# Kernel tuning notes

Hardware: AMD Instinct MI355X
Metric: run time of the kernel (lower is better)

## Reference

```python
import jax, jax.numpy as jnp
import numpy as np

B, L = 4096, 200
G_DIM, L_DIM, A_DIM, H = 64, 64, 8, 32
MAX_ACTION = 1.0


def _init(k, shape, fan_in):
    bound = 1.0 / np.sqrt(fan_in)
    return jax.random.uniform(k, shape, jnp.float32, -bound, bound)


def setup_inputs() -> dict:
    key = jax.random.key(0)
    ks = jax.random.split(key, 16)
    return dict(
        global_states=jax.random.normal(ks[0], (B, G_DIM), jnp.float32),
        local_states=jax.random.normal(ks[1], (B, L, L_DIM), jnp.float32),
        W_w=_init(ks[2], (H, G_DIM), G_DIM), W_b=_init(ks[3], (H,), G_DIM),
        U_w=_init(ks[4], (H, L_DIM), L_DIM), U_b=_init(ks[5], (H,), L_DIM),
        att_w=_init(ks[6], (1, 2 * H), 2 * H), att_b=_init(ks[7], (1,), 2 * H),
        l1_w=_init(ks[8], (256, 2 * H), 2 * H), l1_b=_init(ks[9], (256,), 2 * H),
        l2_w=_init(ks[10], (256, 256), 256), l2_b=_init(ks[11], (256,), 256),
        l3_w=_init(ks[12], (A_DIM, 256), 256), l3_b=_init(ks[13], (A_DIM,), 256),
    )


def reference(global_states, local_states, W_w, W_b, U_w, U_b,
              att_w, att_b, l1_w, l1_b, l2_w, l2_b, l3_w, l3_b):
    h = W_w.shape[0]  # 32
    wg = global_states @ W_w.T + W_b                              # [B,H]
    ul = jnp.einsum('bld,hd->blh', local_states, U_w) + U_b       # [B,L,H]
    # att input row0 = cat(wg, wg); rows 1..L = cat(wg, ul)
    a_g, a_l = att_w[0, :h], att_w[0, h:]
    g_term = wg @ a_g                                             # [B]
    s0 = jax.nn.leaky_relu(g_term + wg @ a_l + att_b[0])          # [B]
    sl = jax.nn.leaky_relu(g_term[:, None] + ul @ a_l + att_b[0]) # [B,L]
    # normalize by sum (not softmax), matching torch.div(score, score.sum())
    total = s0 + sl.sum(axis=1)                                   # [B]
    n0 = s0 / total                                               # [B]
    nl = sl / total[:, None]                                      # [B,L]
    agg_local = jnp.einsum('bl,blh->bh', nl, ul)                  # [B,H]
    states = jax.nn.relu(jnp.concatenate([n0[:, None] * wg, agg_local], axis=1))  # [B,2H]
    a = jax.nn.relu(states @ l1_w.T + l1_b)
    a = jax.nn.relu(a @ l2_w.T + l2_b)
    a = jax.nn.sigmoid(a @ l3_w.T + l3_b)
    return MAX_ACTION * a
```

## Files before the change

kernel.cpp:

```cpp
#include <hip/hip_runtime.h>
#include <math.h>

#define BB 4096
#define LL 200
#define HH 32
#define RR 8

__global__ __launch_bounds__(256) void stream_pool_kernel(
    const float* __restrict__ gs,
    const float* __restrict__ ls,
    const float* __restrict__ W_w, const float* __restrict__ W_b,
    const float* __restrict__ U_w, const float* __restrict__ U_b,
    const float* __restrict__ att_w, const float* __restrict__ att_b,
    float* __restrict__ states)
{
    __shared__ float c_lds[4 * 64];
    __shared__ float y_lds[4 * 64];

    const int tid  = threadIdx.x;
    const int lane = tid & 63;
    const int wid  = tid >> 6;
    const int b    = blockIdx.x * 4 + wid;

    const int h    = lane & 31;
    const int half = lane >> 5;
    const int q    = lane & 15;
    const int lg   = lane >> 4;

    const float4* g4 = (const float4*)(gs + (size_t)b * 64);
    const float4* W4 = (const float4*)(W_w);
    float wg = (half == 0) ? W_b[h] : 0.f;
    #pragma unroll
    for (int dd = 0; dd < 8; ++dd) {
        float4 gv = g4[half * 8 + dd];
        float4 wv = W4[h * 16 + half * 8 + dd];
        wg += gv.x * wv.x + gv.y * wv.y + gv.z * wv.z + gv.w * wv.w;
    }
    wg += __shfl_xor(wg, 32);

    float gt = wg * att_w[h];
    float t2 = wg * att_w[HH + h];
    #pragma unroll
    for (int m = 1; m < 32; m <<= 1) {
        gt += __shfl_xor(gt, m);
        t2 += __shfl_xor(t2, m);
    }
    const float attb = att_b[0];
    const float lin0 = gt + t2 + attb;
    const float s0   = (lin0 > 0.f) ? lin0 : 0.01f * lin0;

    float c = 0.f;
    float ubal = 0.f;
    #pragma unroll
    for (int hh = 0; hh < HH; ++hh) {
        const float alh = att_w[HH + hh];
        c    += alh * U_w[hh * 64 + lane];
        ubal += alh * U_b[hh];
    }
    c_lds[wid * 64 + lane] = c;
    __syncthreads();
    const float4 cq = *(const float4*)&c_lds[wid * 64 + 4 * q];
    const float base = gt + ubal + attb;

    const float4* xs = (const float4*)(ls + (size_t)b * (LL * 64));
    const int idx0 = lg * 16 + q;
    float4 yx = make_float4(0.f, 0.f, 0.f, 0.f);
    float Sacc = 0.f;

    float4 bufA[4], bufB[4];
    #pragma unroll
    for (int i = 0; i < 4; ++i) bufA[i] = xs[idx0 + i * 64];

    #pragma unroll
    for (int g = 0; g < 13; ++g) {
        float4* curb = (g & 1) ? bufB : bufA;
        float4* nxtb = (g & 1) ? bufA : bufB;
        #pragma unroll
        for (int i = 0; i < 4; ++i) {
            const int t = (g + 1) * 4 + i;
            if (t < 50) nxtb[i] = xs[idx0 + t * 64];
        }
        #pragma unroll
        for (int i = 0; i < 4; ++i) {
            const int t = g * 4 + i;
            if (t < 50) {
                float4 X = curb[i];
                float p = X.x * cq.x + X.y * cq.y + X.z * cq.z + X.w * cq.w;
                p += __shfl_xor(p, 1);
                p += __shfl_xor(p, 2);
                p += __shfl_xor(p, 4);
                p += __shfl_xor(p, 8);
                const float linv = p + base;
                const float sl = (linv > 0.f) ? linv : 0.01f * linv;
                yx.x += sl * X.x;
                yx.y += sl * X.y;
                yx.z += sl * X.z;
                yx.w += sl * X.w;
                Sacc += sl;
            }
        }
    }

    #pragma unroll
    for (int m = 16; m < 64; m <<= 1) {
        yx.x += __shfl_xor(yx.x, m);
        yx.y += __shfl_xor(yx.y, m);
        yx.z += __shfl_xor(yx.z, m);
        yx.w += __shfl_xor(yx.w, m);
        Sacc += __shfl_xor(Sacc, m);
    }
    if (lane < 16) *(float4*)&y_lds[wid * 64 + 4 * q] = yx;
    __syncthreads();

    float V = (half == 0) ? (U_b[h] * Sacc) : 0.f;
    const float4* U4 = (const float4*)U_w;
    const float4* y4 = (const float4*)&y_lds[wid * 64];
    #pragma unroll
    for (int dd = 0; dd < 8; ++dd) {
        float4 uv = U4[h * 16 + half * 8 + dd];
        float4 yv = y4[half * 8 + dd];
        V += uv.x * yv.x + uv.y * yv.y + uv.z * yv.z + uv.w * yv.w;
    }
    V += __shfl_xor(V, 32);

    const float total = s0 + Sacc;
    const float n0    = s0 / total;
    const float outv  = (lane < 32) ? (n0 * wg) : (V / total);
    states[(size_t)b * 64 + lane] = fmaxf(outv, 0.f);
}

__global__ __launch_bounds__(256) void mlp_kernel(
    const float* __restrict__ states,
    const float* __restrict__ l1_w, const float* __restrict__ l1_b,
    const float* __restrict__ l2_w, const float* __restrict__ l2_b,
    const float* __restrict__ l3_w, const float* __restrict__ l3_b,
    float* __restrict__ out)
{
    __shared__ float s_w[256 * 33];
    __shared__ __align__(16) float s_x [RR * 64];
    __shared__ __align__(16) float s_a1[RR * 256];
    __shared__ __align__(16) float s_a2[RR * 260];

    const int tid = threadIdx.x;
    const int b0  = blockIdx.x * RR;

    const float4* st4 = (const float4*)(states + (size_t)b0 * 64);
    if (tid < RR * 16) ((float4*)s_x)[tid] = st4[tid];

    float acc[RR];

    {
        const float bias = l1_b[tid];
        #pragma unroll
        for (int r = 0; r < RR; ++r) acc[r] = bias;

        for (int kc = 0; kc < 2; ++kc) {
            __syncthreads();
            #pragma unroll
            for (int i = 0; i < 8; ++i) {
                const int f   = tid + i * 256;
                const int j   = f >> 3;
                const int sg  = f & 7;
                const float4 v = *(const float4*)(l1_w + j * 64 + kc * 32 + sg * 4);
                float* dst = &s_w[j * 33 + sg * 4];
                dst[0] = v.x; dst[1] = v.y; dst[2] = v.z; dst[3] = v.w;
            }
            __syncthreads();
            #pragma unroll
            for (int d4 = 0; d4 < 8; ++d4) {
                const float w0 = s_w[tid * 33 + d4 * 4 + 0];
                const float w1 = s_w[tid * 33 + d4 * 4 + 1];
                const float w2 = s_w[tid * 33 + d4 * 4 + 2];
                const float w3 = s_w[tid * 33 + d4 * 4 + 3];
                #pragma unroll
                for (int r = 0; r < RR; ++r) {
                    const float4 xv = *(const float4*)&s_x[r * 64 + kc * 32 + d4 * 4];
                    acc[r] += w0 * xv.x + w1 * xv.y + w2 * xv.z + w3 * xv.w;
                }
            }
        }
        #pragma unroll
        for (int r = 0; r < RR; ++r)
            s_a1[r * 256 + tid] = fmaxf(acc[r], 0.f);
    }

    {
        const float bias = l2_b[tid];
        #pragma unroll
        for (int r = 0; r < RR; ++r) acc[r] = bias;

        for (int kc = 0; kc < 8; ++kc) {
            __syncthreads();
            #pragma unroll
            for (int i = 0; i < 8; ++i) {
                const int f   = tid + i * 256;
                const int j   = f >> 3;
                const int sg  = f & 7;
                const float4 v = *(const float4*)(l2_w + j * 256 + kc * 32 + sg * 4);
                float* dst = &s_w[j * 33 + sg * 4];
                dst[0] = v.x; dst[1] = v.y; dst[2] = v.z; dst[3] = v.w;
            }
            __syncthreads();
            #pragma unroll
            for (int d4 = 0; d4 < 8; ++d4) {
                const float w0 = s_w[tid * 33 + d4 * 4 + 0];
                const float w1 = s_w[tid * 33 + d4 * 4 + 1];
                const float w2 = s_w[tid * 33 + d4 * 4 + 2];
                const float w3 = s_w[tid * 33 + d4 * 4 + 3];
                #pragma unroll
                for (int r = 0; r < RR; ++r) {
                    const float4 av = *(const float4*)&s_a1[r * 256 + kc * 32 + d4 * 4];
                    acc[r] += w0 * av.x + w1 * av.y + w2 * av.z + w3 * av.w;
                }
            }
        }
        #pragma unroll
        for (int r = 0; r < RR; ++r)
            s_a2[r * 260 + tid] = fmaxf(acc[r], 0.f);
    }
    __syncthreads();

    if (tid < RR * 8) {
        const int r = tid >> 3, o = tid & 7;
        float a = l3_b[o];
        const float4* wr4 = (const float4*)(l3_w + o * 256);
        const float4* a4  = (const float4*)&s_a2[r * 260];
        #pragma unroll 8
        for (int k = 0; k < 64; ++k) {
            const float4 av = a4[k];
            const float4 wv = wr4[k];
            a += av.x * wv.x + av.y * wv.y + av.z * wv.z + av.w * wv.w;
        }
        out[(size_t)(b0 + r) * 8 + o] = 1.f / (1.f + __expf(-a));
    }
}

extern "C" void kernel_launch(void* const* d_in, const int* in_sizes, int n_in,
                              void* d_out, int out_size, void* d_ws, size_t ws_size,
                              hipStream_t stream)
{
    const float* gs    = (const float*)d_in[0];
    const float* ls    = (const float*)d_in[1];
    const float* W_w   = (const float*)d_in[2];
    const float* W_b   = (const float*)d_in[3];
    const float* U_w   = (const float*)d_in[4];
    const float* U_b   = (const float*)d_in[5];
    const float* att_w = (const float*)d_in[6];
    const float* att_b = (const float*)d_in[7];
    const float* l1_w  = (const float*)d_in[8];
    const float* l1_b  = (const float*)d_in[9];
    const float* l2_w  = (const float*)d_in[10];
    const float* l2_b  = (const float*)d_in[11];
    const float* l3_w  = (const float*)d_in[12];
    const float* l3_b  = (const float*)d_in[13];

    float* states = (float*)d_ws;

    stream_pool_kernel<<<BB / 4, 256, 0, stream>>>(
        gs, ls, W_w, W_b, U_w, U_b, att_w, att_b, states);
    mlp_kernel<<<BB / RR, 256, 0, stream>>>(
        states, l1_w, l1_b, l2_w, l2_b, l3_w, l3_b, (float*)d_out);
}
```

Before: 373.0 us.

## Stage each batch row in LDS with one block per row for attention pooling

Rewrites the pooling kernel to use one 256-thread block per batch element. The block loads the full 200x64 local-state tile into padded shared memory, then computes scores and the weighted sum from LDS. This replaces the per-wave register-streaming and shuffle-reduction scheme and is meant to spread work over more threads. In exchange it uses about 52KB of LDS per block, which limits occupancy, and adds block-wide syncs and single-thread serial sections.

```diff
diff --git a/kernel.cpp b/kernel.cpp
--- a/kernel.cpp
+++ b/kernel.cpp
@@ -4,9 +4,10 @@
 #define BB 4096
 #define LL 200
 #define HH 32
+#define PITCH 65
 #define RR 8
 
-__global__ __launch_bounds__(256) void stream_pool_kernel(
+__global__ __launch_bounds__(256) void pool_kernel(
     const float* __restrict__ gs,
     const float* __restrict__ ls,
     const float* __restrict__ W_w, const float* __restrict__ W_b,
@@ -14,119 +15,121 @@
     const float* __restrict__ att_w, const float* __restrict__ att_b,
     float* __restrict__ states)
 {
-    __shared__ float c_lds[4 * 64];
-    __shared__ float y_lds[4 * 64];
-
-    const int tid  = threadIdx.x;
-    const int lane = tid & 63;
-    const int wid  = tid >> 6;
-    const int b    = blockIdx.x * 4 + wid;
-
-    const int h    = lane & 31;
-    const int half = lane >> 5;
-    const int q    = lane & 15;
-    const int lg   = lane >> 4;
-
-    const float4* g4 = (const float4*)(gs + (size_t)b * 64);
-    const float4* W4 = (const float4*)(W_w);
-    float wg = (half == 0) ? W_b[h] : 0.f;
+    __shared__ float xT[LL * PITCH];
+    __shared__ float sl_s[LL];
+    __shared__ float ypart[4][64];
+    __shared__ float wg_s[HH];
+    __shared__ float c_s[64];
+    __shared__ float V_s[HH];
+    __shared__ float misc[4];
+
+    const int tid = threadIdx.x;
+    const int b   = blockIdx.x;
+
+    const float4* src = (const float4*)(ls + (size_t)b * (LL * 64));
+    float4 v[13];
     #pragma unroll
-    for (int dd = 0; dd < 8; ++dd) {
-        float4 gv = g4[half * 8 + dd];
-        float4 wv = W4[h * 16 + half * 8 + dd];
-        wg += gv.x * wv.x + gv.y * wv.y + gv.z * wv.z + gv.w * wv.w;
-    }
-    wg += __shfl_xor(wg, 32);
-
-    float gt = wg * att_w[h];
-    float t2 = wg * att_w[HH + h];
+    for (int k = 0; k < 13; ++k) {
+        const int f = tid + (k << 8);
+        if (f < LL * 16) v[k] = src[f];
+    }
+
+    const float attb = att_b[0];
+    if (tid < 64) {
+        float cacc = 0.f, ub = 0.f;
+        #pragma unroll
+        for (int hh = 0; hh < HH; ++hh) {
+            const float alh = att_w[HH + hh];
+            cacc += alh * U_w[hh * 64 + tid];
+            ub   += alh * U_b[hh];
+        }
+        c_s[tid] = cacc;
+        if (tid == 0) misc[0] = ub;
+    } else if (tid < 96) {
+        const int h = tid - 64;
+        float acc = W_b[h];
+        const float* g = gs + (size_t)b * 64;
+        #pragma unroll
+        for (int d = 0; d < 64; ++d)
+            acc += g[d] * W_w[h * 64 + d];
+        wg_s[h] = acc;
+    }
+
     #pragma unroll
-    for (int m = 1; m < 32; m <<= 1) {
-        gt += __shfl_xor(gt, m);
-        t2 += __shfl_xor(t2, m);
-    }
-    const float attb = att_b[0];
-    const float lin0 = gt + t2 + attb;
-    const float s0   = (lin0 > 0.f) ? lin0 : 0.01f * lin0;
-
-    float c = 0.f;
-    float ubal = 0.f;
-    #pragma unroll
-    for (int hh = 0; hh < HH; ++hh) {
-        const float alh = att_w[HH + hh];
-        c    += alh * U_w[hh * 64 + lane];
-        ubal += alh * U_b[hh];
-    }
-    c_lds[wid * 64 + lane] = c;
-    __syncthreads();
-    const float4 cq = *(const float4*)&c_lds[wid * 64 + 4 * q];
-    const float base = gt + ubal + attb;
-
-    const float4* xs = (const float4*)(ls + (size_t)b * (LL * 64));
-    const int idx0 = lg * 16 + q;
-    float4 yx = make_float4(0.f, 0.f, 0.f, 0.f);
-    float Sacc = 0.f;
-
-    float4 bufA[4], bufB[4];
-    #pragma unroll
-    for (int i = 0; i < 4; ++i) bufA[i] = xs[idx0 + i * 64];
-
-    #pragma unroll
-    for (int g = 0; g < 13; ++g) {
-        float4* curb = (g & 1) ? bufB : bufA;
-        float4* nxtb = (g & 1) ? bufA : bufB;
-        #pragma unroll
-        for (int i = 0; i < 4; ++i) {
-            const int t = (g + 1) * 4 + i;
-            if (t < 50) nxtb[i] = xs[idx0 + t * 64];
-        }
-        #pragma unroll
-        for (int i = 0; i < 4; ++i) {
-            const int t = g * 4 + i;
-            if (t < 50) {
-                float4 X = curb[i];
-                float p = X.x * cq.x + X.y * cq.y + X.z * cq.z + X.w * cq.w;
-                p += __shfl_xor(p, 1);
-                p += __shfl_xor(p, 2);
-                p += __shfl_xor(p, 4);
-                p += __shfl_xor(p, 8);
-                const float linv = p + base;
-                const float sl = (linv > 0.f) ? linv : 0.01f * linv;
-                yx.x += sl * X.x;
-                yx.y += sl * X.y;
-                yx.z += sl * X.z;
-                yx.w += sl * X.w;
-                Sacc += sl;
-            }
-        }
-    }
-
-    #pragma unroll
-    for (int m = 16; m < 64; m <<= 1) {
-        yx.x += __shfl_xor(yx.x, m);
-        yx.y += __shfl_xor(yx.y, m);
-        yx.z += __shfl_xor(yx.z, m);
-        yx.w += __shfl_xor(yx.w, m);
-        Sacc += __shfl_xor(Sacc, m);
-    }
-    if (lane < 16) *(float4*)&y_lds[wid * 64 + 4 * q] = yx;
-    __syncthreads();
-
-    float V = (half == 0) ? (U_b[h] * Sacc) : 0.f;
-    const float4* U4 = (const float4*)U_w;
-    const float4* y4 = (const float4*)&y_lds[wid * 64];
-    #pragma unroll
-    for (int dd = 0; dd < 8; ++dd) {
-        float4 uv = U4[h * 16 + half * 8 + dd];
-        float4 yv = y4[half * 8 + dd];
-        V += uv.x * yv.x + uv.y * yv.y + uv.z * yv.z + uv.w * yv.w;
-    }
-    V += __shfl_xor(V, 32);
-
-    const float total = s0 + Sacc;
-    const float n0    = s0 / total;
-    const float outv  = (lane < 32) ? (n0 * wg) : (V / total);
-    states[(size_t)b * 64 + lane] = fmaxf(outv, 0.f);
+    for (int k = 0; k < 13; ++k) {
+        const int f = tid + (k << 8);
+        if (f < LL * 16) {
+            const int l  = f >> 4;
+            const int c4 = (f & 15) << 2;
+            float* dst = &xT[l * PITCH + c4];
+            dst[0] = v[k].x; dst[1] = v[k].y; dst[2] = v[k].z; dst[3] = v[k].w;
+        }
+    }
+    __syncthreads();
+
+    if (tid == 0) {
+        float gt = 0.f, t2 = 0.f;
+        #pragma unroll
+        for (int h = 0; h < HH; ++h) {
+            gt += wg_s[h] * att_w[h];
+            t2 += wg_s[h] * att_w[HH + h];
+        }
+        const float lin0 = gt + t2 + attb;
+        misc[1] = gt;
+        misc[2] = (lin0 > 0.f) ? lin0 : 0.01f * lin0;
+    }
+    __syncthreads();
+
+    if (tid < LL) {
+        const float* row = &xT[tid * PITCH];
+        float p = 0.f;
+        #pragma unroll 16
+        for (int d = 0; d < 64; ++d)
+            p += row[d] * c_s[d];
+        const float lin = p + misc[1] + misc[0] + attb;
+        sl_s[tid] = (lin > 0.f) ? lin : 0.01f * lin;
+    }
+    __syncthreads();
+
+    {
+        const int qd = tid >> 6;
+        const int d  = tid & 63;
+        float yp = 0.f;
+        #pragma unroll 10
+        for (int i = 0; i < 50; ++i) {
+            const int l = qd * 50 + i;
+            yp += sl_s[l] * xT[l * PITCH + d];
+        }
+        ypart[qd][d] = yp;
+    }
+    if (tid < 64) {
+        float sp = sl_s[tid] + sl_s[tid + 64] + sl_s[tid + 128];
+        if (tid < 8) sp += sl_s[tid + 192];
+        #pragma unroll
+        for (int m = 1; m < 64; m <<= 1)
+            sp += __shfl_xor(sp, m);
+        if (tid == 0) misc[3] = sp;
+    }
+    __syncthreads();
+
+    if (tid < 64) {
+        const float yd = ypart[0][tid] + ypart[1][tid] +
+                         ypart[2][tid] + ypart[3][tid];
+        ypart[0][tid] = yd;
+        const float S = misc[3];
+        if (tid < HH) {
+            float V = U_b[tid] * S;
+            #pragma unroll 8
+            for (int d = 0; d < 64; ++d)
+                V += U_w[tid * 64 + d] * ypart[0][d];
+            V_s[tid] = V;
+        }
+        const float s0    = misc[2];
+        const float total = s0 + S;
+        const float outv  = (tid < HH) ? ((s0 / total) * wg_s[tid])
+                                       : (V_s[tid - HH] / total);
+        states[(size_t)b * 64 + tid] = fmaxf(outv, 0.f);
+    }
 }
 
 __global__ __launch_bounds__(256) void mlp_kernel(
@@ -158,9 +161,9 @@
             __syncthreads();
             #pragma unroll
             for (int i = 0; i < 8; ++i) {
-                const int f   = tid + i * 256;
-                const int j   = f >> 3;
-                const int sg  = f & 7;
+                const int f  = tid + i * 256;
+                const int j  = f >> 3;
+                const int sg = f & 7;
                 const float4 v = *(const float4*)(l1_w + j * 64 + kc * 32 + sg * 4);
                 float* dst = &s_w[j * 33 + sg * 4];
                 dst[0] = v.x; dst[1] = v.y; dst[2] = v.z; dst[3] = v.w;
@@ -193,9 +196,9 @@
             __syncthreads();
             #pragma unroll
             for (int i = 0; i < 8; ++i) {
-                const int f   = tid + i * 256;
-                const int j   = f >> 3;
-                const int sg  = f & 7;
+                const int f  = tid + i * 256;
+                const int j  = f >> 3;
+                const int sg = f & 7;
                 const float4 v = *(const float4*)(l2_w + j * 256 + kc * 32 + sg * 4);
                 float* dst = &s_w[j * 33 + sg * 4];
                 dst[0] = v.x; dst[1] = v.y; dst[2] = v.z; dst[3] = v.w;
@@ -256,7 +259,7 @@
 
     float* states = (float*)d_ws;
 
-    stream_pool_kernel<<<BB / 4, 256, 0, stream>>>(
+    pool_kernel<<<BB, 256, 0, stream>>>(
         gs, ls, W_w, W_b, U_w, U_b, att_w, att_b, states);
     mlp_kernel<<<BB / RR, 256, 0, stream>>>(
         states, l1_w, l1_b, l2_w, l2_b, l3_w, l3_b, (float*)d_out);
```

Measured after the change: 362.0 us. -2.9%, faster.
